# Optimization experiments

Measured on AMD Instinct MI355X. Metric: run time of the kernel, lower is better.

## Reference

```python
import jax, jax.numpy as jnp
import numpy as np

N, E, F, H, L, G, C = 50000, 800000, 64, 128, 4, 64, 10
GAMMA = 10.0  # Gaussian RBF width for centers in (0,1)
CENTERS = jnp.linspace(0.0, 1.0, H)


def _ssp(v):
    # shifted softplus, SchNet's nonlinearity
    return jax.nn.softplus(v) - 0.6931472


def setup_inputs() -> dict:
    key = jax.random.key(0)
    ks = jax.random.split(key, 20)

    def w(k, shape, fan_in):
        return (jax.random.normal(k, shape, dtype=jnp.float32) / np.sqrt(fan_in)).astype(jnp.float32)

    x = jax.random.normal(ks[0], (N, F), dtype=jnp.float32)
    edge_dist = jax.random.uniform(ks[1], (E,), dtype=jnp.float32)
    edge_src = jax.random.randint(ks[2], (E,), 0, N, dtype=jnp.int32)
    edge_dst = jax.random.randint(ks[3], (E,), 0, N, dtype=jnp.int32)
    graph_ids = jnp.sort(jax.random.randint(ks[4], (N,), 0, G, dtype=jnp.int32))

    return {
        "x": x, "edge_dist": edge_dist,
        "edge_src": edge_src, "edge_dst": edge_dst, "graph_ids": graph_ids,
        # first-layer node projection F->H, remaining layers H->H (stacked)
        "W1_0": w(ks[5], (F, H), F), "b1_0": jnp.zeros((H,), jnp.float32),
        "W1_rest": w(ks[6], (L - 1, H, H), H), "b1_rest": jnp.zeros((L - 1, H), jnp.float32),
        # filter-generating MLP on RBF features, per layer
        "Wf1": w(ks[7], (L, H, H), H), "bf1": jnp.zeros((L, H), jnp.float32),
        "Wf2": w(ks[8], (L, H, H), H), "bf2": jnp.zeros((L, H), jnp.float32),
        # output projection per layer
        "W2": w(ks[9], (L, H, H), H), "b2": jnp.zeros((L, H), jnp.float32),
        # readout FC
        "fc_w": w(ks[10], (H, C), H), "fc_b": jnp.zeros((C,), jnp.float32),
    }


def _schnet_conv(x, rbf, src, dst, W1, b1, Wf1, bf1, Wf2, bf2, W2, b2):
    # CFConv: project nodes, gate gathered source features with a distance
    # filter, scatter-sum to destinations, project out.
    filt = _ssp(rbf @ Wf1 + bf1) @ Wf2 + bf2          # [E, H]
    h = x @ W1 + b1                                    # [N, H]
    msg = h[src] * filt                                # [E, H] gather + gate
    agg = jax.ops.segment_sum(msg, dst, num_segments=N)  # [N, H] scatter-sum
    return agg @ W2 + b2


def reference(x, edge_dist, edge_src, edge_dst, graph_ids,
              W1_0, b1_0, W1_rest, b1_rest, Wf1, bf1, Wf2, bf2, W2, b2,
              fc_w, fc_b):
    # Gaussian radial basis expansion of edge distances, shared across layers
    rbf = jnp.exp(-GAMMA * (edge_dist[:, None] - CENTERS) ** 2)  # [E, H]

    h = jax.nn.relu(_schnet_conv(x, rbf, edge_src, edge_dst,
                                 W1_0, b1_0, Wf1[0], bf1[0], Wf2[0], bf2[0],
                                 W2[0], b2[0]))
    for i in range(L - 1):
        h = jax.nn.relu(_schnet_conv(h, rbf, edge_src, edge_dst,
                                     W1_rest[i], b1_rest[i],
                                     Wf1[i + 1], bf1[i + 1],
                                     Wf2[i + 1], bf2[i + 1],
                                     W2[i + 1], b2[i + 1]))

    # dgl.mean_nodes: per-graph mean over nodes
    sums = jax.ops.segment_sum(h, graph_ids, num_segments=G)           # [G, H]
    cnts = jax.ops.segment_sum(jnp.ones((N,), h.dtype), graph_ids, num_segments=G)
    pooled = sums / jnp.maximum(cnts, 1.0)[:, None]

    logits = pooled @ fc_w + fc_b                                       # [G, C]
    return jax.nn.log_softmax(logits, axis=1)
```

## Files before the change

kernel.cpp:

```cpp
#include <hip/hip_runtime.h>
#include <math.h>

#define NN 50000
#define EE 800000
#define FF 64
#define HH 128
#define LL 4
#define GG 64
#define CC 10
#define TT 512
#define TTP 513
#define BD 64
#define ABLK 1024
#define EPB 782
#define SEGC 192
#define SUBB 96
#define SRW 6250

#define PB_CVTW 8
#define PB_TAB ((TT / 16) * LL)
#define PB_CVTX (NN * FF / 4 / 256)
#define PB_PART ABLK

#define SCB (8 * SUBB)
#define GEMMB (NN / 16)

typedef unsigned short ushort_t;
typedef unsigned int uint_t;

typedef short s8v __attribute__((ext_vector_type(8)));
typedef float f32x4 __attribute__((ext_vector_type(4)));

__device__ inline ushort_t f2bf(float f) {
  uint_t u = __float_as_uint(f);
  uint_t r = (u + 0x7FFFu + ((u >> 16) & 1u)) >> 16;
  return (ushort_t)r;
}
__device__ inline float bf_lo(uint_t pair) { return __uint_as_float(pair << 16); }
__device__ inline float bf_hi(uint_t pair) { return __uint_as_float(pair & 0xFFFF0000u); }
__device__ inline float bf1f(ushort_t v) { return __uint_as_float(((uint_t)v) << 16); }

__global__ __launch_bounds__(256) void prep(
    const float* __restrict__ x, ushort_t* __restrict__ xb,
    const float* __restrict__ W1_0, const float* __restrict__ W1_rest,
    const float* __restrict__ W2, ushort_t* __restrict__ wt,
    const float* __restrict__ Wf1, const float* __restrict__ bf1,
    const float* __restrict__ Wf2, const float* __restrict__ bf2,
    ushort_t* __restrict__ tables,
    const int* __restrict__ dst, const int* __restrict__ src,
    const float* __restrict__ dist,
    uint2* __restrict__ seg, int* __restrict__ segcnt, int* __restrict__ bcnt,
    const int* __restrict__ gid, int* __restrict__ gcnt, float* __restrict__ gsum) {
  __shared__ float rbf[16][HH];
  __shared__ float hid[16][HH];
  __shared__ int lcnt[8];
  int tid = threadIdx.x;
  int b = blockIdx.x;

  if (b < PB_CVTW) {
    int mid = b;
    const float* srcm; int K;
    if (mid == 0) { srcm = W1_0; K = FF; }
    else if (mid < 4) { srcm = W1_rest + (size_t)(mid - 1) * HH * HH; K = HH; }
    else { srcm = W2 + (size_t)(mid - 4) * HH * HH; K = HH; }
    ushort_t* dstm = wt + (size_t)mid * HH * HH;
    for (int idx = tid; idx < K * HH; idx += 256) {
      int k = idx >> 7, n = idx & 127;
      dstm[n * K + k] = f2bf(srcm[idx]);
    }
  } else if (b < PB_CVTW + PB_TAB) {
    int bb = b - PB_CVTW;
    int l = bb & 3;
    int tb = (bb >> 2) * 16;
    int j = tid & 127;
    float c = j * (1.0f / (HH - 1));
#pragma unroll
    for (int tt2 = 0; tt2 < 16; ++tt2) {
      float d = (tb + tt2) * (1.0f / (TT - 1));
      float dd = d - c;
      rbf[tt2][j] = expf(-10.0f * dd * dd);
    }
    __syncthreads();
    const float* W1f = Wf1 + (size_t)l * HH * HH;
    float s[16];
    float bb1 = bf1[l * HH + j];
#pragma unroll
    for (int tt2 = 0; tt2 < 16; ++tt2) s[tt2] = bb1;
    for (int k = 0; k < HH; ++k) {
      float wk = W1f[(size_t)k * HH + j];
#pragma unroll
      for (int tt2 = 0; tt2 < 16; ++tt2) s[tt2] += rbf[tt2][k] * wk;
    }
#pragma unroll
    for (int tt2 = 0; tt2 < 16; ++tt2)
      hid[tt2][j] = fmaxf(s[tt2], 0.f) + log1pf(expf(-fabsf(s[tt2]))) - 0.6931472f;
    __syncthreads();
    const float* W2f = Wf2 + (size_t)l * HH * HH;
    float bb2 = bf2[l * HH + j];
#pragma unroll
    for (int tt2 = 0; tt2 < 16; ++tt2) s[tt2] = bb2;
    for (int k = 0; k < HH; ++k) {
      float wk = W2f[(size_t)k * HH + j];
#pragma unroll
      for (int tt2 = 0; tt2 < 16; ++tt2) s[tt2] += hid[tt2][k] * wk;
    }
    if (tid < 128) {
#pragma unroll
      for (int tt2 = 0; tt2 < 16; ++tt2)
        tables[((size_t)l * TTP + 1 + tb + tt2) * HH + j] = f2bf(s[tt2]);
    }
  } else if (b < PB_CVTW + PB_TAB + PB_CVTX) {
    int i = (b - PB_CVTW - PB_TAB) * 256 + tid;
    const float4* x4 = (const float4*)x;
    float4 v = x4[i];
    union { ushort_t us[4]; uint2 u; } pk;
    pk.us[0] = f2bf(v.x); pk.us[1] = f2bf(v.y); pk.us[2] = f2bf(v.z); pk.us[3] = f2bf(v.w);
    *(uint2*)&xb[i * 4] = pk.u;
  } else if (b < PB_CVTW + PB_TAB + PB_CVTX + PB_PART) {
    int pb = b - PB_CVTW - PB_TAB - PB_CVTX;
    if (tid < 8) lcnt[tid] = 0;
    int z = pb * 49 + tid;
    if (tid < 49 && z < NN) bcnt[z] = 0;
    __syncthreads();
    int e0 = pb * EPB;
    int e1 = min(e0 + EPB, EE);
    for (int e = e0 + tid; e < e1; e += 256) {
      int d = __builtin_nontemporal_load(dst + e);
      int s = __builtin_nontemporal_load(src + e);
      float di = __builtin_nontemporal_load(dist + e);
      float u = di * (float)(TT - 1);
      int t0 = (int)(fminf(fmaxf(u, 0.f), (float)(TT - 1)) + 0.5f);
      if (t0 > TT - 1) t0 = TT - 1;
      int r = d / SRW;
      int pos = atomicAdd(&lcnt[r], 1);
      if (pos < SEGC)
        seg[((size_t)(r << 10) + pb) * SEGC + pos] =
            make_uint2((uint_t)d, ((uint_t)s << 10) | (uint_t)(t0 + 1));
    }
    __syncthreads();
    if (tid < 8) segcnt[(tid << 10) + pb] = min(lcnt[tid], SEGC);
  } else {
    for (int i = tid; i < GG * HH; i += 256) gsum[i] = 0.f;
    for (int i = tid; i < LL * HH; i += 256)
      tables[(size_t)(i >> 7) * TTP * HH + (i & 127)] = 0;
    if (tid < GG) {
      int g = tid;
      int lo = 0, hi = NN;
      while (lo < hi) { int m = (lo + hi) >> 1; if (gid[m] < g) lo = m + 1; else hi = m; }
      int b0 = lo;
      lo = 0; hi = NN;
      int g1 = g + 1;
      while (lo < hi) { int m = (lo + hi) >> 1; if (gid[m] < g1) lo = m + 1; else hi = m; }
      gcnt[g] = lo - b0;
    }
  }
}

__global__ __launch_bounds__(256) void scatter_gemm1(
    const uint2* __restrict__ seg, const int* __restrict__ segcnt,
    int* __restrict__ bcnt, uint_t* __restrict__ epad,
    const ushort_t* __restrict__ xb, const ushort_t* __restrict__ wt,
    const float* __restrict__ b1_0, ushort_t* __restrict__ pbuf) {
  int tid = threadIdx.x;
  if (blockIdx.x < SCB) {
    int r = blockIdx.x & 7;
    int sub = blockIdx.x >> 3;
    for (int b = sub; b < ABLK; b += SUBB) {
      int cnt = segcnt[(r << 10) + b];
      const uint_t* sp = (const uint_t*)(seg + ((size_t)(r << 10) + b) * SEGC);
      for (int i = tid; i < cnt; i += 256) {
        uint_t ex = __builtin_nontemporal_load(sp + i * 2);
        uint_t ey = __builtin_nontemporal_load(sp + i * 2 + 1);
        int slot = atomicAdd(&bcnt[ex], 1);
        if (slot < BD) epad[(size_t)ex * BD + slot] = ey;
      }
    }
  } else {
    int tile = blockIdx.x - SCB;
    int lane = tid & 63, wave = tid >> 6, m = lane & 15, quad = lane >> 4;
    int rowbase = tile * 16, colbase = wave * 32;
    const ushort_t* arow = xb + (size_t)(rowbase + m) * FF;
    const ushort_t* brow0 = wt + (size_t)(colbase + m) * FF;
    const ushort_t* brow1 = wt + (size_t)(colbase + 16 + m) * FF;
    f32x4 acc0 = {0.f, 0.f, 0.f, 0.f};
    f32x4 acc1 = {0.f, 0.f, 0.f, 0.f};
    for (int kc = 0; kc < FF; kc += 32) {
      int k = kc + quad * 8;
      union { uint4 u; s8v v; } a, b0, b1;
      a.u  = *(const uint4*)(arow + k);
      b0.u = *(const uint4*)(brow0 + k);
      b1.u = *(const uint4*)(brow1 + k);
      acc0 = __builtin_amdgcn_mfma_f32_16x16x32_bf16(a.v, b0.v, acc0, 0, 0, 0);
      acc1 = __builtin_amdgcn_mfma_f32_16x16x32_bf16(a.v, b1.v, acc1, 0, 0, 0);
    }
    float bb0 = b1_0[colbase + m];
    float bb1 = b1_0[colbase + 16 + m];
#pragma unroll
    for (int reg = 0; reg < 4; ++reg) {
      int row = rowbase + quad * 4 + reg;
      pbuf[(size_t)row * HH + colbase + m] = f2bf(acc0[reg] + bb0);
      pbuf[(size_t)row * HH + colbase + 16 + m] = f2bf(acc1[reg] + bb1);
    }
  }
}

__global__ __launch_bounds__(256) void fused_layer(
    const ushort_t* __restrict__ pIn, const ushort_t* __restrict__ table,
    const uint_t* __restrict__ epad, const int* __restrict__ bcnt,
    const ushort_t* __restrict__ WT2, const float* __restrict__ b2l,
    const ushort_t* __restrict__ WT1, const float* __restrict__ b1l,
    ushort_t* __restrict__ OUT, int last) {
  __shared__ ushort_t At[16 * 128];
  __shared__ ushort_t T[16 * 128];
  int tid = threadIdx.x;
  int lane = tid & 63;
  int wv = tid >> 6;
  int tile = blockIdx.x;
  const uint_t* pu = (const uint_t*)pIn;
  const uint_t* tu = (const uint_t*)table;

  int baseV = tile * 16 + wv * 4;
  uint_t ed[4];
  float ax[4], ay[4];
  int B = 0;
#pragma unroll
  for (int i = 0; i < 4; ++i) {
    int n = min(bcnt[baseV + i], BD);
    ed[i] = (lane < n) ? epad[(size_t)(baseV + i) * BD + lane] : 0u;
    int nb = (n + 3) >> 2;
    B = max(B, nb);
    ax[i] = 0.f; ay[i] = 0.f;
  }
  for (int b = 0; b < B; ++b) {
    int j4 = b << 2;
#pragma unroll
    for (int i = 0; i < 4; ++i) {
#pragma unroll
      for (int k = 0; k < 4; ++k) {
        uint_t e = (uint_t)__builtin_amdgcn_readlane((int)ed[i], j4 + k);
        uint_t pv = pu[(size_t)(e >> 10) * 64 + lane];
        uint_t fv = tu[(size_t)(e & 1023u) * 64 + lane];
        ax[i] += bf_lo(pv) * bf_lo(fv);
        ay[i] += bf_hi(pv) * bf_hi(fv);
      }
    }
  }
#pragma unroll
  for (int i = 0; i < 4; ++i) {
    int r = wv * 4 + i;
    uint_t packed = (uint_t)f2bf(ax[i]) | ((uint_t)f2bf(ay[i]) << 16);
    ((uint_t*)At)[r * 64 + (((lane >> 2) ^ r) << 2) + (lane & 3)] = packed;
  }
  __syncthreads();
  int m = lane & 15, quad = lane >> 4;
  int rowbase = tile * 16, colbase = wv * 32;
  {
    const ushort_t* brow0 = WT2 + (size_t)(colbase + m) * HH;
    const ushort_t* brow1 = WT2 + (size_t)(colbase + 16 + m) * HH;
    f32x4 acc0 = {0.f, 0.f, 0.f, 0.f};
    f32x4 acc1 = {0.f, 0.f, 0.f, 0.f};
    for (int kc = 0; kc < HH; kc += 32) {
      int k = kc + quad * 8;
      int g = k >> 3;
      union { uint4 u; s8v v; } a, b0, b1;
      a.u = *(const uint4*)&At[m * 128 + ((g ^ m) << 3)];
      b0.u = *(const uint4*)(brow0 + k);
      b1.u = *(const uint4*)(brow1 + k);
      acc0 = __builtin_amdgcn_mfma_f32_16x16x32_bf16(a.v, b0.v, acc0, 0, 0, 0);
      acc1 = __builtin_amdgcn_mfma_f32_16x16x32_bf16(a.v, b1.v, acc1, 0, 0, 0);
    }
    float bb0 = b2l[colbase + m];
    float bb1 = b2l[colbase + 16 + m];
    if (last) {
#pragma unroll
      for (int reg = 0; reg < 4; ++reg) {
        int row = rowbase + quad * 4 + reg;
        OUT[(size_t)row * HH + colbase + m] = f2bf(fmaxf(acc0[reg] + bb0, 0.f));
        OUT[(size_t)row * HH + colbase + 16 + m] = f2bf(fmaxf(acc1[reg] + bb1, 0.f));
      }
      return;
    }
#pragma unroll
    for (int reg = 0; reg < 4; ++reg) {
      int r = quad * 4 + reg;
      float v0 = fmaxf(acc0[reg] + bb0, 0.f);
      float v1 = fmaxf(acc1[reg] + bb1, 0.f);
      int c0 = colbase + m, c1 = colbase + 16 + m;
      T[r * 128 + (((c0 >> 3) ^ r) << 3) + (c0 & 7)] = f2bf(v0);
      T[r * 128 + (((c1 >> 3) ^ r) << 3) + (c1 & 7)] = f2bf(v1);
    }
  }
  __syncthreads();
  {
    const ushort_t* brow0 = WT1 + (size_t)(colbase + m) * HH;
    const ushort_t* brow1 = WT1 + (size_t)(colbase + 16 + m) * HH;
    f32x4 acc0 = {0.f, 0.f, 0.f, 0.f};
    f32x4 acc1 = {0.f, 0.f, 0.f, 0.f};
    for (int kc = 0; kc < HH; kc += 32) {
      int k0 = kc + quad * 8;
      int g = k0 >> 3;
      union { uint4 u; s8v v; } a, b0, b1;
      a.u = *(const uint4*)&T[m * 128 + ((g ^ m) << 3)];
      b0.u = *(const uint4*)(brow0 + k0);
      b1.u = *(const uint4*)(brow1 + k0);
      acc0 = __builtin_amdgcn_mfma_f32_16x16x32_bf16(a.v, b0.v, acc0, 0, 0, 0);
      acc1 = __builtin_amdgcn_mfma_f32_16x16x32_bf16(a.v, b1.v, acc1, 0, 0, 0);
    }
    float bb0 = b1l[colbase + m];
    float bb1 = b1l[colbase + 16 + m];
#pragma unroll
    for (int reg = 0; reg < 4; ++reg) {
      int row = rowbase + quad * 4 + reg;
      OUT[(size_t)row * HH + colbase + m] = f2bf(acc0[reg] + bb0);
      OUT[(size_t)row * HH + colbase + 16 + m] = f2bf(acc1[reg] + bb1);
    }
  }
}

__global__ __launch_bounds__(128) void pool_kernel(const ushort_t* __restrict__ h, const int* __restrict__ gid,
                                                   float* __restrict__ gsum) {
  int j = threadIdx.x;
  int i0 = blockIdx.x * 128;
  int i1 = min(i0 + 128, NN);
  if (i0 >= NN) return;
  float acc = 0.f;
  int gcur = gid[i0];
  for (int i = i0; i < i1; ++i) {
    int g = gid[i];
    if (g != gcur) {
      atomicAdd(&gsum[gcur * HH + j], acc);
      acc = 0.f;
      gcur = g;
    }
    acc += bf1f(h[(size_t)i * HH + j]);
  }
  atomicAdd(&gsum[gcur * HH + j], acc);
}

__global__ __launch_bounds__(128) void final_kernel(const float* __restrict__ gsum, const int* __restrict__ gcnt,
                                                    const float* __restrict__ fc_w, const float* __restrict__ fc_b,
                                                    float* __restrict__ out) {
  int g = blockIdx.x, j = threadIdx.x;
  __shared__ float pooled[HH];
  __shared__ float logits[CC];
  __shared__ float lse;
  float cnt = fmaxf((float)gcnt[g], 1.0f);
  pooled[j] = gsum[g * HH + j] / cnt;
  __syncthreads();
  if (j < CC) {
    float s = fc_b[j];
    for (int k = 0; k < HH; ++k) s += pooled[k] * fc_w[k * CC + j];
    logits[j] = s;
  }
  __syncthreads();
  if (j == 0) {
    float m = -1e30f;
    for (int c = 0; c < CC; ++c) m = fmaxf(m, logits[c]);
    float s = 0.f;
    for (int c = 0; c < CC; ++c) s += expf(logits[c] - m);
    lse = m + logf(s);
  }
  __syncthreads();
  if (j < CC) out[g * CC + j] = logits[j] - lse;
}

extern "C" void kernel_launch(void* const* d_in, const int* in_sizes, int n_in,
                              void* d_out, int out_size, void* d_ws, size_t ws_size,
                              hipStream_t stream) {
  const float* x       = (const float*)d_in[0];
  const float* edist   = (const float*)d_in[1];
  const int*   esrc    = (const int*)d_in[2];
  const int*   edst    = (const int*)d_in[3];
  const int*   gid     = (const int*)d_in[4];
  const float* W1_0    = (const float*)d_in[5];
  const float* b1_0    = (const float*)d_in[6];
  const float* W1_rest = (const float*)d_in[7];
  const float* b1_rest = (const float*)d_in[8];
  const float* Wf1     = (const float*)d_in[9];
  const float* bf1     = (const float*)d_in[10];
  const float* Wf2     = (const float*)d_in[11];
  const float* bf2     = (const float*)d_in[12];
  const float* W2      = (const float*)d_in[13];
  const float* b2      = (const float*)d_in[14];
  const float* fc_w    = (const float*)d_in[15];
  const float* fc_b    = (const float*)d_in[16];
  float* out = (float*)d_out;

  char* ws = (char*)d_ws;
  size_t o = 0;
  auto alloc = [&](size_t bytes) {
    void* p = ws + o;
    o += (bytes + 255) & ~(size_t)255;
    return p;
  };
  ushort_t* tables = (ushort_t*)alloc(sizeof(ushort_t) * (size_t)LL * TTP * HH);
  ushort_t* xb     = (ushort_t*)alloc(sizeof(ushort_t) * (size_t)NN * FF);
  ushort_t* wt     = (ushort_t*)alloc(sizeof(ushort_t) * 8 * HH * HH);
  ushort_t* pbuf   = (ushort_t*)alloc(sizeof(ushort_t) * (size_t)NN * HH);
  ushort_t* pbuf2  = (ushort_t*)alloc(sizeof(ushort_t) * (size_t)NN * HH);
  ushort_t* hbuf   = (ushort_t*)alloc(sizeof(ushort_t) * (size_t)NN * HH);
  int*      bcnt   = (int*)alloc(sizeof(int) * NN);
  uint_t*   epad   = (uint_t*)alloc(sizeof(uint_t) * (size_t)NN * BD);
  uint2*    seg    = (uint2*)alloc(sizeof(uint2) * (size_t)8 * ABLK * SEGC);
  int*      segcnt = (int*)alloc(sizeof(int) * 8 * ABLK);
  float*    gsum   = (float*)alloc(sizeof(float) * GG * HH);
  int*      gcnt   = (int*)alloc(sizeof(int) * GG);

  const int prepBlocks = PB_CVTW + PB_TAB + PB_CVTX + PB_PART + 1;
  prep<<<prepBlocks, 256, 0, stream>>>(x, xb, W1_0, W1_rest, W2, wt,
                                       Wf1, bf1, Wf2, bf2, tables,
                                       edst, esrc, edist, seg, segcnt, bcnt,
                                       gid, gcnt, gsum);
  scatter_gemm1<<<SCB + GEMMB, 256, 0, stream>>>(seg, segcnt, bcnt, epad,
                                                 xb, wt, b1_0, pbuf);

  ushort_t* pIn = pbuf;
  ushort_t* pOut = pbuf2;
  for (int l = 0; l < LL; ++l) {
    int last = (l == LL - 1);
    fused_layer<<<GEMMB, 256, 0, stream>>>(
        pIn, tables + (size_t)l * TTP * HH, epad, bcnt,
        wt + (size_t)(4 + l) * HH * HH, b2 + (size_t)l * HH,
        last ? nullptr : (wt + (size_t)(1 + l) * HH * HH),
        last ? nullptr : (b1_rest + (size_t)l * HH),
        last ? hbuf : pOut, last);
    ushort_t* tmp = pIn; pIn = pOut; pOut = tmp;
  }

  pool_kernel<<<(NN + 127) / 128, 128, 0, stream>>>(hbuf, gid, gsum);
  final_kernel<<<GG, 128, 0, stream>>>(gsum, gcnt, fc_w, fc_b, out);
}
```

Measured before the change: 405.9 us.

## Quantize per-layer node projections to int8 with per-row scales for gathers

The node projection buffers that are gathered per edge are now stored as int8 with a per-row float scale instead of bf16, computed with a shared-memory atomicMax over each row. The edge gather loop is restructured so each wave processes two edges at once: half-waves each handle one edge, loading 4 int8 values and 4 bf16 filter values per lane, and the halves are combined with a cross-lane shuffle. The aim is to halve the gathered bytes per edge and raise memory-level parallelism in the bandwidth-bound aggregation. The cost is added quantization error, an extra scale load per edge, and an extra block barrier in the epilogue.

```diff
diff --git a/kernel.cpp b/kernel.cpp
--- a/kernel.cpp
+++ b/kernel.cpp
@@ -160,7 +160,9 @@
     const uint2* __restrict__ seg, const int* __restrict__ segcnt,
     int* __restrict__ bcnt, uint_t* __restrict__ epad,
     const ushort_t* __restrict__ xb, const ushort_t* __restrict__ wt,
-    const float* __restrict__ b1_0, ushort_t* __restrict__ pbuf) {
+    const float* __restrict__ b1_0, char* __restrict__ q8Out,
+    float* __restrict__ sclOut) {
+  __shared__ uint_t rmaxL[16];
   int tid = threadIdx.x;
   if (blockIdx.x < SCB) {
     int r = blockIdx.x & 7;
@@ -176,6 +178,7 @@
       }
     }
   } else {
+    if (tid < 16) rmaxL[tid] = 0u;
     int tile = blockIdx.x - SCB;
     int lane = tid & 63, wave = tid >> 6, m = lane & 15, quad = lane >> 4;
     int rowbase = tile * 16, colbase = wave * 32;
@@ -195,61 +198,89 @@
     }
     float bb0 = b1_0[colbase + m];
     float bb1 = b1_0[colbase + 16 + m];
+    float v0r[4], v1r[4];
 #pragma unroll
     for (int reg = 0; reg < 4; ++reg) {
-      int row = rowbase + quad * 4 + reg;
-      pbuf[(size_t)row * HH + colbase + m] = f2bf(acc0[reg] + bb0);
-      pbuf[(size_t)row * HH + colbase + 16 + m] = f2bf(acc1[reg] + bb1);
-    }
+      v0r[reg] = acc0[reg] + bb0;
+      v1r[reg] = acc1[reg] + bb1;
+      int r = quad * 4 + reg;
+      atomicMax(&rmaxL[r], __float_as_uint(fmaxf(fabsf(v0r[reg]), fabsf(v1r[reg]))));
+    }
+    __syncthreads();
+#pragma unroll
+    for (int reg = 0; reg < 4; ++reg) {
+      int r = quad * 4 + reg;
+      int row = rowbase + r;
+      float inv = 127.0f / fmaxf(__uint_as_float(rmaxL[r]), 1e-30f);
+      q8Out[(size_t)row * HH + colbase + m] = (char)(int)rintf(v0r[reg] * inv);
+      q8Out[(size_t)row * HH + colbase + 16 + m] = (char)(int)rintf(v1r[reg] * inv);
+    }
+    if (tid < 16) sclOut[rowbase + tid] = __uint_as_float(rmaxL[tid]) * (1.0f / 127.0f);
   }
 }
 
 __global__ __launch_bounds__(256) void fused_layer(
-    const ushort_t* __restrict__ pIn, const ushort_t* __restrict__ table,
+    const char* __restrict__ q8In, const float* __restrict__ sclIn,
+    const ushort_t* __restrict__ table,
     const uint_t* __restrict__ epad, const int* __restrict__ bcnt,
     const ushort_t* __restrict__ WT2, const float* __restrict__ b2l,
     const ushort_t* __restrict__ WT1, const float* __restrict__ b1l,
-    ushort_t* __restrict__ OUT, int last) {
+    char* __restrict__ q8Out, float* __restrict__ sclOut,
+    ushort_t* __restrict__ hbuf, int last) {
   __shared__ ushort_t At[16 * 128];
   __shared__ ushort_t T[16 * 128];
+  __shared__ uint_t rmaxL[16];
   int tid = threadIdx.x;
   int lane = tid & 63;
   int wv = tid >> 6;
   int tile = blockIdx.x;
-  const uint_t* pu = (const uint_t*)pIn;
-  const uint_t* tu = (const uint_t*)table;
+  int l32 = lane & 31;
+  if (tid < 16) rmaxL[tid] = 0u;
 
   int baseV = tile * 16 + wv * 4;
   uint_t ed[4];
-  float ax[4], ay[4];
-  int B = 0;
+  float a0[4], a1[4], a2[4], a3[4];
+  int B2 = 0;
 #pragma unroll
   for (int i = 0; i < 4; ++i) {
     int n = min(bcnt[baseV + i], BD);
     ed[i] = (lane < n) ? epad[(size_t)(baseV + i) * BD + lane] : 0u;
-    int nb = (n + 3) >> 2;
-    B = max(B, nb);
-    ax[i] = 0.f; ay[i] = 0.f;
-  }
-  for (int b = 0; b < B; ++b) {
-    int j4 = b << 2;
+    B2 = max(B2, (n + 1) >> 1);
+    a0[i] = 0.f; a1[i] = 0.f; a2[i] = 0.f; a3[i] = 0.f;
+  }
+  for (int p = 0; p < B2; ++p) {
 #pragma unroll
     for (int i = 0; i < 4; ++i) {
-#pragma unroll
-      for (int k = 0; k < 4; ++k) {
-        uint_t e = (uint_t)__builtin_amdgcn_readlane((int)ed[i], j4 + k);
-        uint_t pv = pu[(size_t)(e >> 10) * 64 + lane];
-        uint_t fv = tu[(size_t)(e & 1023u) * 64 + lane];
-        ax[i] += bf_lo(pv) * bf_lo(fv);
-        ay[i] += bf_hi(pv) * bf_hi(fv);
-      }
+      uint_t eA = (uint_t)__builtin_amdgcn_readlane((int)ed[i], 2 * p);
+      uint_t eB = (uint_t)__builtin_amdgcn_readlane((int)ed[i], 2 * p + 1);
+      float ssA = sclIn[eA >> 10];
+      float ssB = sclIn[eB >> 10];
+      uint_t e = (lane < 32) ? eA : eB;
+      float ss = (lane < 32) ? ssA : ssB;
+      uint_t pv = *(const uint_t*)(q8In + ((size_t)(e >> 10) << 7) + (l32 << 2));
+      uint2 fp = *(const uint2*)((const char*)table + ((size_t)(e & 1023u) << 8) + (l32 << 3));
+      float q0 = (float)(int)(signed char)(pv & 0xffu);
+      float q1 = (float)(int)(signed char)((pv >> 8) & 0xffu);
+      float q2 = (float)(int)(signed char)((pv >> 16) & 0xffu);
+      float q3 = (float)(int)(signed char)(pv >> 24);
+      a0[i] += (q0 * ss) * bf_lo(fp.x);
+      a1[i] += (q1 * ss) * bf_hi(fp.x);
+      a2[i] += (q2 * ss) * bf_lo(fp.y);
+      a3[i] += (q3 * ss) * bf_hi(fp.y);
     }
   }
 #pragma unroll
   for (int i = 0; i < 4; ++i) {
+    a0[i] += __shfl_xor(a0[i], 32);
+    a1[i] += __shfl_xor(a1[i], 32);
+    a2[i] += __shfl_xor(a2[i], 32);
+    a3[i] += __shfl_xor(a3[i], 32);
     int r = wv * 4 + i;
-    uint_t packed = (uint_t)f2bf(ax[i]) | ((uint_t)f2bf(ay[i]) << 16);
-    ((uint_t*)At)[r * 64 + (((lane >> 2) ^ r) << 2) + (lane & 3)] = packed;
+    int d0 = l32 * 2, d1 = l32 * 2 + 1;
+    ((uint_t*)At)[r * 64 + (((d0 >> 2) ^ r) << 2) + (d0 & 3)] =
+        (uint_t)f2bf(a0[i]) | ((uint_t)f2bf(a1[i]) << 16);
+    ((uint_t*)At)[r * 64 + (((d1 >> 2) ^ r) << 2) + (d1 & 3)] =
+        (uint_t)f2bf(a2[i]) | ((uint_t)f2bf(a3[i]) << 16);
   }
   __syncthreads();
   int m = lane & 15, quad = lane >> 4;
@@ -275,8 +306,8 @@
 #pragma unroll
       for (int reg = 0; reg < 4; ++reg) {
         int row = rowbase + quad * 4 + reg;
-        OUT[(size_t)row * HH + colbase + m] = f2bf(fmaxf(acc0[reg] + bb0, 0.f));
-        OUT[(size_t)row * HH + colbase + 16 + m] = f2bf(fmaxf(acc1[reg] + bb1, 0.f));
+        hbuf[(size_t)row * HH + colbase + m] = f2bf(fmaxf(acc0[reg] + bb0, 0.f));
+        hbuf[(size_t)row * HH + colbase + 16 + m] = f2bf(fmaxf(acc1[reg] + bb1, 0.f));
       }
       return;
     }
@@ -308,12 +339,24 @@
     }
     float bb0 = b1l[colbase + m];
     float bb1 = b1l[colbase + 16 + m];
+    float v0r[4], v1r[4];
 #pragma unroll
     for (int reg = 0; reg < 4; ++reg) {
-      int row = rowbase + quad * 4 + reg;
-      OUT[(size_t)row * HH + colbase + m] = f2bf(acc0[reg] + bb0);
-      OUT[(size_t)row * HH + colbase + 16 + m] = f2bf(acc1[reg] + bb1);
-    }
+      v0r[reg] = acc0[reg] + bb0;
+      v1r[reg] = acc1[reg] + bb1;
+      int r = quad * 4 + reg;
+      atomicMax(&rmaxL[r], __float_as_uint(fmaxf(fabsf(v0r[reg]), fabsf(v1r[reg]))));
+    }
+    __syncthreads();
+#pragma unroll
+    for (int reg = 0; reg < 4; ++reg) {
+      int r = quad * 4 + reg;
+      int row = rowbase + r;
+      float inv = 127.0f / fmaxf(__uint_as_float(rmaxL[r]), 1e-30f);
+      q8Out[(size_t)row * HH + colbase + m] = (char)(int)rintf(v0r[reg] * inv);
+      q8Out[(size_t)row * HH + colbase + 16 + m] = (char)(int)rintf(v1r[reg] * inv);
+    }
+    if (tid < 16) sclOut[rowbase + tid] = __uint_as_float(rmaxL[tid]) * (1.0f / 127.0f);
   }
 }
 
@@ -396,8 +439,10 @@
   ushort_t* tables = (ushort_t*)alloc(sizeof(ushort_t) * (size_t)LL * TTP * HH);
   ushort_t* xb     = (ushort_t*)alloc(sizeof(ushort_t) * (size_t)NN * FF);
   ushort_t* wt     = (ushort_t*)alloc(sizeof(ushort_t) * 8 * HH * HH);
-  ushort_t* pbuf   = (ushort_t*)alloc(sizeof(ushort_t) * (size_t)NN * HH);
-  ushort_t* pbuf2  = (ushort_t*)alloc(sizeof(ushort_t) * (size_t)NN * HH);
+  char*     q8a    = (char*)alloc(sizeof(char) * (size_t)NN * HH);
+  char*     q8b    = (char*)alloc(sizeof(char) * (size_t)NN * HH);
+  float*    scla   = (float*)alloc(sizeof(float) * (size_t)NN);
+  float*    sclb   = (float*)alloc(sizeof(float) * (size_t)NN);
   ushort_t* hbuf   = (ushort_t*)alloc(sizeof(ushort_t) * (size_t)NN * HH);
   int*      bcnt   = (int*)alloc(sizeof(int) * NN);
   uint_t*   epad   = (uint_t*)alloc(sizeof(uint_t) * (size_t)NN * BD);
@@ -412,19 +457,22 @@
                                        edst, esrc, edist, seg, segcnt, bcnt,
                                        gid, gcnt, gsum);
   scatter_gemm1<<<SCB + GEMMB, 256, 0, stream>>>(seg, segcnt, bcnt, epad,
-                                                 xb, wt, b1_0, pbuf);
-
-  ushort_t* pIn = pbuf;
-  ushort_t* pOut = pbuf2;
+                                                 xb, wt, b1_0, q8a, scla);
+
+  const char* pIn = q8a;
+  const float* sIn = scla;
+  char* pOut = q8b;
+  float* sOut = sclb;
   for (int l = 0; l < LL; ++l) {
     int last = (l == LL - 1);
     fused_layer<<<GEMMB, 256, 0, stream>>>(
-        pIn, tables + (size_t)l * TTP * HH, epad, bcnt,
+        pIn, sIn, tables + (size_t)l * TTP * HH, epad, bcnt,
         wt + (size_t)(4 + l) * HH * HH, b2 + (size_t)l * HH,
         last ? nullptr : (wt + (size_t)(1 + l) * HH * HH),
         last ? nullptr : (b1_rest + (size_t)l * HH),
-        last ? hbuf : pOut, last);
-    ushort_t* tmp = pIn; pIn = pOut; pOut = tmp;
+        pOut, sOut, hbuf, last);
+    const char* tp = pIn; pIn = pOut; pOut = (char*)tp;
+    const float* ts = sIn; sIn = sOut; sOut = (float*)ts;
   }
 
   pool_kernel<<<(NN + 127) / 128, 128, 0, stream>>>(hbuf, gid, gsum);
```

Measured after the change: 408.2 us. No clear change (+0.5%).

## Use fp16 gathered operands, 512-thread fused layer blocks, batch gather loads

Applied to the files above, without the earlier changes.

Node projections and filter tables are now stored as fp16 instead of bf16, which gives the gathered products more mantissa precision. The fused layer kernel moves from 4 to 8 waves per block. Each wave now handles 2 destination nodes instead of 4 and 16 output columns instead of 32. The gather loop issues all loads for a chunk before any FMA, so more loads are in flight. The trade-offs are a wider fp16 conversion path and possible overflow if values leave the fp16 range; the MFMA stages also get less work per wave.

```diff
diff --git a/kernel.cpp b/kernel.cpp
--- a/kernel.cpp
+++ b/kernel.cpp
@@ -36,9 +36,19 @@
   uint_t r = (u + 0x7FFFu + ((u >> 16) & 1u)) >> 16;
   return (ushort_t)r;
 }
-__device__ inline float bf_lo(uint_t pair) { return __uint_as_float(pair << 16); }
-__device__ inline float bf_hi(uint_t pair) { return __uint_as_float(pair & 0xFFFF0000u); }
 __device__ inline float bf1f(ushort_t v) { return __uint_as_float(((uint_t)v) << 16); }
+
+__device__ inline ushort_t f2h(float f) {
+  union { _Float16 h[2]; ushort_t us[2]; } c;
+  c.h[0] = (_Float16)f;
+  return c.us[0];
+}
+__device__ inline float h_lo(uint_t u) {
+  union { uint_t w; _Float16 h[2]; } c; c.w = u; return (float)c.h[0];
+}
+__device__ inline float h_hi(uint_t u) {
+  union { uint_t w; _Float16 h[2]; } c; c.w = u; return (float)c.h[1];
+}
 
 __global__ __launch_bounds__(256) void prep(
     const float* __restrict__ x, ushort_t* __restrict__ xb,
@@ -107,7 +117,7 @@
     if (tid < 128) {
 #pragma unroll
       for (int tt2 = 0; tt2 < 16; ++tt2)
-        tables[((size_t)l * TTP + 1 + tb + tt2) * HH + j] = f2bf(s[tt2]);
+        tables[((size_t)l * TTP + 1 + tb + tt2) * HH + j] = f2h(s[tt2]);
     }
   } else if (b < PB_CVTW + PB_TAB + PB_CVTX) {
     int i = (b - PB_CVTW - PB_TAB) * 256 + tid;
@@ -198,13 +208,13 @@
 #pragma unroll
     for (int reg = 0; reg < 4; ++reg) {
       int row = rowbase + quad * 4 + reg;
-      pbuf[(size_t)row * HH + colbase + m] = f2bf(acc0[reg] + bb0);
-      pbuf[(size_t)row * HH + colbase + 16 + m] = f2bf(acc1[reg] + bb1);
-    }
-  }
-}
-
-__global__ __launch_bounds__(256) void fused_layer(
+      pbuf[(size_t)row * HH + colbase + m] = f2h(acc0[reg] + bb0);
+      pbuf[(size_t)row * HH + colbase + 16 + m] = f2h(acc1[reg] + bb1);
+    }
+  }
+}
+
+__global__ __launch_bounds__(512) void fused_layer(
     const ushort_t* __restrict__ pIn, const ushort_t* __restrict__ table,
     const uint_t* __restrict__ epad, const int* __restrict__ bcnt,
     const ushort_t* __restrict__ WT2, const float* __restrict__ b2l,
@@ -219,64 +229,63 @@
   const uint_t* pu = (const uint_t*)pIn;
   const uint_t* tu = (const uint_t*)table;
 
-  int baseV = tile * 16 + wv * 4;
-  uint_t ed[4];
-  float ax[4], ay[4];
+  int baseV = tile * 16 + wv * 2;
+  uint_t ed[2];
+  float ax[2], ay[2];
   int B = 0;
 #pragma unroll
-  for (int i = 0; i < 4; ++i) {
+  for (int i = 0; i < 2; ++i) {
     int n = min(bcnt[baseV + i], BD);
     ed[i] = (lane < n) ? epad[(size_t)(baseV + i) * BD + lane] : 0u;
-    int nb = (n + 3) >> 2;
-    B = max(B, nb);
+    B = max(B, (n + 3) >> 2);
     ax[i] = 0.f; ay[i] = 0.f;
   }
-  for (int b = 0; b < B; ++b) {
-    int j4 = b << 2;
-#pragma unroll
-    for (int i = 0; i < 4; ++i) {
+  for (int c = 0; c < B; ++c) {
+    uint_t pv[2][4], fv[2][4];
+#pragma unroll
+    for (int i = 0; i < 2; ++i) {
 #pragma unroll
       for (int k = 0; k < 4; ++k) {
-        uint_t e = (uint_t)__builtin_amdgcn_readlane((int)ed[i], j4 + k);
-        uint_t pv = pu[(size_t)(e >> 10) * 64 + lane];
-        uint_t fv = tu[(size_t)(e & 1023u) * 64 + lane];
-        ax[i] += bf_lo(pv) * bf_lo(fv);
-        ay[i] += bf_hi(pv) * bf_hi(fv);
+        uint_t e = (uint_t)__builtin_amdgcn_readlane((int)ed[i], c * 4 + k);
+        pv[i][k] = pu[(size_t)(e >> 10) * 64 + lane];
+        fv[i][k] = tu[(size_t)(e & 1023u) * 64 + lane];
       }
     }
-  }
-#pragma unroll
-  for (int i = 0; i < 4; ++i) {
-    int r = wv * 4 + i;
+#pragma unroll
+    for (int i = 0; i < 2; ++i) {
+#pragma unroll
+      for (int k = 0; k < 4; ++k) {
+        ax[i] += h_lo(pv[i][k]) * h_lo(fv[i][k]);
+        ay[i] += h_hi(pv[i][k]) * h_hi(fv[i][k]);
+      }
+    }
+  }
+#pragma unroll
+  for (int i = 0; i < 2; ++i) {
+    int r = wv * 2 + i;
     uint_t packed = (uint_t)f2bf(ax[i]) | ((uint_t)f2bf(ay[i]) << 16);
     ((uint_t*)At)[r * 64 + (((lane >> 2) ^ r) << 2) + (lane & 3)] = packed;
   }
   __syncthreads();
   int m = lane & 15, quad = lane >> 4;
-  int rowbase = tile * 16, colbase = wv * 32;
+  int rowbase = tile * 16, colbase = wv * 16;
   {
     const ushort_t* brow0 = WT2 + (size_t)(colbase + m) * HH;
-    const ushort_t* brow1 = WT2 + (size_t)(colbase + 16 + m) * HH;
     f32x4 acc0 = {0.f, 0.f, 0.f, 0.f};
-    f32x4 acc1 = {0.f, 0.f, 0.f, 0.f};
     for (int kc = 0; kc < HH; kc += 32) {
       int k = kc + quad * 8;
       int g = k >> 3;
-      union { uint4 u; s8v v; } a, b0, b1;
+      union { uint4 u; s8v v; } a, b0;
       a.u = *(const uint4*)&At[m * 128 + ((g ^ m) << 3)];
       b0.u = *(const uint4*)(brow0 + k);
-      b1.u = *(const uint4*)(brow1 + k);
       acc0 = __builtin_amdgcn_mfma_f32_16x16x32_bf16(a.v, b0.v, acc0, 0, 0, 0);
-      acc1 = __builtin_amdgcn_mfma_f32_16x16x32_bf16(a.v, b1.v, acc1, 0, 0, 0);
     }
     float bb0 = b2l[colbase + m];
-    float bb1 = b2l[colbase + 16 + m];
     if (last) {
 #pragma unroll
       for (int reg = 0; reg < 4; ++reg) {
         int row = rowbase + quad * 4 + reg;
         OUT[(size_t)row * HH + colbase + m] = f2bf(fmaxf(acc0[reg] + bb0, 0.f));
-        OUT[(size_t)row * HH + colbase + 16 + m] = f2bf(fmaxf(acc1[reg] + bb1, 0.f));
       }
       return;
     }
@@ -284,35 +293,27 @@
     for (int reg = 0; reg < 4; ++reg) {
       int r = quad * 4 + reg;
       float v0 = fmaxf(acc0[reg] + bb0, 0.f);
-      float v1 = fmaxf(acc1[reg] + bb1, 0.f);
-      int c0 = colbase + m, c1 = colbase + 16 + m;
+      int c0 = colbase + m;
       T[r * 128 + (((c0 >> 3) ^ r) << 3) + (c0 & 7)] = f2bf(v0);
-      T[r * 128 + (((c1 >> 3) ^ r) << 3) + (c1 & 7)] = f2bf(v1);
     }
   }
   __syncthreads();
   {
     const ushort_t* brow0 = WT1 + (size_t)(colbase + m) * HH;
-    const ushort_t* brow1 = WT1 + (size_t)(colbase + 16 + m) * HH;
     f32x4 acc0 = {0.f, 0.f, 0.f, 0.f};
-    f32x4 acc1 = {0.f, 0.f, 0.f, 0.f};
     for (int kc = 0; kc < HH; kc += 32) {
       int k0 = kc + quad * 8;
       int g = k0 >> 3;
-      union { uint4 u; s8v v; } a, b0, b1;
+      union { uint4 u; s8v v; } a, b0;
       a.u = *(const uint4*)&T[m * 128 + ((g ^ m) << 3)];
       b0.u = *(const uint4*)(brow0 + k0);
-      b1.u = *(const uint4*)(brow1 + k0);
       acc0 = __builtin_amdgcn_mfma_f32_16x16x32_bf16(a.v, b0.v, acc0, 0, 0, 0);
-      acc1 = __builtin_amdgcn_mfma_f32_16x16x32_bf16(a.v, b1.v, acc1, 0, 0, 0);
     }
     float bb0 = b1l[colbase + m];
-    float bb1 = b1l[colbase + 16 + m];
 #pragma unroll
     for (int reg = 0; reg < 4; ++reg) {
       int row = rowbase + quad * 4 + reg;
-      OUT[(size_t)row * HH + colbase + m] = f2bf(acc0[reg] + bb0);
-      OUT[(size_t)row * HH + colbase + 16 + m] = f2bf(acc1[reg] + bb1);
+      OUT[(size_t)row * HH + colbase + m] = f2h(acc0[reg] + bb0);
     }
   }
 }
@@ -418,7 +419,7 @@
   ushort_t* pOut = pbuf2;
   for (int l = 0; l < LL; ++l) {
     int last = (l == LL - 1);
-    fused_layer<<<GEMMB, 256, 0, stream>>>(
+    fused_layer<<<GEMMB, 512, 0, stream>>>(
         pIn, tables + (size_t)l * TTP * HH, epad, bcnt,
         wt + (size_t)(4 + l) * HH * HH, b2 + (size_t)l * HH,
         last ? nullptr : (wt + (size_t)(1 + l) * HH * HH),
```

New measurement: 397.8 us. 2.0% less time.
